# Kernel optimization log

Measured on AMD Instinct MI355X. Metric: run time of the kernel, lower is better.

Reference implementation:

```python
import jax, jax.numpy as jnp
import numpy as np

N_NODES = 100000
N_EDGES = 1600000
N_GRAPHS = 64
HID = 128
N_EXPERTS = 8
IN_DIM = 4


def setup_inputs() -> dict:
    key = jax.random.key(0)
    ks = jax.random.split(key, 12)
    atomic_numbers = jax.random.uniform(ks[0], (N_NODES,), dtype=jnp.float32) * 80.0
    pos = jax.random.normal(ks[1], (N_NODES, 3), dtype=jnp.float32)
    edge_index = jax.random.randint(ks[2], (2, N_EDGES), 0, N_NODES, dtype=jnp.int64)
    batch = jnp.sort(jax.random.randint(ks[3], (N_NODES,), 0, N_GRAPHS, dtype=jnp.int64))
    s1 = 1.0 / np.sqrt(IN_DIM)
    s2 = 1.0 / np.sqrt(HID)
    W1 = jax.random.uniform(ks[4], (IN_DIM, HID), jnp.float32, -s1, s1)
    b1 = jnp.zeros((HID,), jnp.float32)
    W2 = jax.random.uniform(ks[5], (HID, HID), jnp.float32, -s2, s2)
    b2 = jnp.zeros((HID,), jnp.float32)
    Wlin = jax.random.uniform(ks[6], (HID, N_EXPERTS), jnp.float32, -s2, s2)
    blin = jax.random.uniform(ks[7], (N_EXPERTS,), jnp.float32, -s2, s2)
    return {"atomic_numbers": atomic_numbers, "pos": pos, "edge_index": edge_index,
            "batch": batch, "W1": W1, "b1": b1, "W2": W2, "b2": b2,
            "Wlin": Wlin, "blin": blin}


def _gcn_conv(x, W, b, src, dst, deg_inv_sqrt, n_nodes):
    # PyG GCNConv: x' = W x; aggregate deg^-1/2[src]*deg^-1/2[dst] * x'[src] into dst; + bias
    h = x @ W  # [N, out]
    norm = deg_inv_sqrt[src] * deg_inv_sqrt[dst]  # [E+N]
    msg = h[src] * norm[:, None]  # gathered, normalized messages
    out = jax.ops.segment_sum(msg, dst, num_segments=n_nodes)
    return out + b


def reference(atomic_numbers, pos, edge_index, batch, W1, b1, W2, b2, Wlin, blin):
    n = atomic_numbers.shape[0]
    x = jnp.concatenate([atomic_numbers[:, None], pos], axis=-1)  # [N, 4]
    # add self-loops (GCNConv default add_self_loops=True)
    loop = jnp.arange(n, dtype=edge_index.dtype)
    src = jnp.concatenate([edge_index[0], loop])
    dst = jnp.concatenate([edge_index[1], loop])
    deg = jax.ops.segment_sum(jnp.ones_like(dst, dtype=jnp.float32), dst, num_segments=n)
    deg_inv_sqrt = jnp.where(deg > 0, jax.lax.rsqrt(jnp.maximum(deg, 1e-12)), 0.0)
    x = _gcn_conv(x, W1, b1, src, dst, deg_inv_sqrt, n)
    x = jax.nn.relu(x)
    # dropout p=0.5 is identity in eval mode
    x = _gcn_conv(x, W2, b2, src, dst, deg_inv_sqrt, n)
    x = x @ Wlin + blin  # [N, num_experts]
    # global_mean_pool over graph ids
    sums = jax.ops.segment_sum(x, batch, num_segments=N_GRAPHS)
    cnts = jax.ops.segment_sum(jnp.ones((n,), jnp.float32), batch, num_segments=N_GRAPHS)
    pooled = sums / jnp.maximum(cnts, 1.0)[:, None]
    return jax.nn.log_softmax(pooled, axis=1)
```

## Files before the change

### kernel.cpp

```cpp
#include <hip/hip_runtime.h>
#include <math.h>

#define HID 128
#define NEXP 8
#define NGRAPH 64
#define EPC 2048
#define EPT 8
#define MAXB 512
#define NXC 8
#define NREP 8
#define NPS 8
#define HALF 128
#define STAGE_CAP 4096

__device__ inline unsigned short f2bf(float f) {
    unsigned u = __float_as_uint(f);
    u += 0x7FFF + ((u >> 16) & 1);
    return (unsigned short)(u >> 16);
}
__device__ inline unsigned packbf(float lo, float hi) {
    return (unsigned)f2bf(lo) | ((unsigned)f2bf(hi) << 16);
}
__device__ inline float bflo(unsigned u) { return __uint_as_float(u << 16); }
__device__ inline float bfhi(unsigned u) { return __uint_as_float(u & 0xFFFF0000u); }

__global__ void k_init0(float* __restrict__ pool, float* __restrict__ pcnt,
                        const float* __restrict__ W2, const float* __restrict__ Wlin,
                        const float* __restrict__ b2, float* __restrict__ C,
                        float* __restrict__ bb2, int* __restrict__ gcur8,
                        int mregions, int capx) {
    int i = blockIdx.x * 256 + threadIdx.x;
    if (i < mregions) gcur8[i] = i * capx;
    if (i == mregions) gcur8[i] = 0;
    if (i < NREP * NGRAPH * NEXP) pool[i] = 0.0f;
    if (i < NREP * NGRAPH) pcnt[i] = 0.0f;
    int ci = i - NREP * NGRAPH * NEXP;
    if (ci >= 0 && ci < HID * NEXP) {
        int k = ci >> 3, j = ci & 7;
        float s = 0.0f;
        for (int m = 0; m < HID; m++) s += W2[k * HID + m] * Wlin[m * NEXP + j];
        C[ci] = s;
    }
    int bi = ci - HID * NEXP;
    if (bi >= 0 && bi < NEXP) {
        float s = 0.0f;
        for (int m = 0; m < HID; m++) s += b2[m] * Wlin[m * NEXP + bi];
        bb2[bi] = s;
    }
}

__global__ void __launch_bounds__(256) k_binA(
        const int* __restrict__ src, const int* __restrict__ dst,
        int* __restrict__ gcur8, unsigned* __restrict__ binned, int e, int nbuck) {
    __shared__ int h0[MAXB];
    __shared__ int h1[MAXB];
    __shared__ int lstart[MAXB];
    __shared__ int lcur[MAXB];
    __shared__ int gbase[MAXB];
    __shared__ int wtot[4];
    __shared__ unsigned packed[EPC];
    __shared__ unsigned short sbkt[EPC];
    int c = blockIdx.x, t = threadIdx.x;
    int w = t >> 6, lane = t & 63;
    int x = c & (NXC - 1);
    int start = c * EPC;
    int m = e - start < EPC ? e - start : EPC;

    int d[EPT], sv[EPT];
    if (m == EPC) {
        const int4* d4 = (const int4*)(dst + start);
        const int4* s4 = (const int4*)(src + start);
#pragma unroll
        for (int q = 0; q < EPT / 4; q++) {
            int4 dd4 = d4[(EPT / 4) * t + q];
            int4 ss4 = s4[(EPT / 4) * t + q];
            d[4 * q + 0] = dd4.x; d[4 * q + 1] = dd4.y;
            d[4 * q + 2] = dd4.z; d[4 * q + 3] = dd4.w;
            sv[4 * q + 0] = ss4.x; sv[4 * q + 1] = ss4.y;
            sv[4 * q + 2] = ss4.z; sv[4 * q + 3] = ss4.w;
        }
    } else {
#pragma unroll
        for (int j = 0; j < EPT; j++) {
            int idx = t * EPT + j;
            if (idx < m) { d[j] = dst[start + idx]; sv[j] = src[start + idx]; }
        }
    }
    int* hm = (w < 2) ? h0 : h1;
    h0[t] = 0; h0[t + 256] = 0;
    h1[t] = 0; h1[t + 256] = 0;
    __syncthreads();
#pragma unroll
    for (int j = 0; j < EPT; j++)
        if (t * EPT + j < m) atomicAdd(&hm[d[j] >> 8], 1);
    __syncthreads();
    int v0 = h0[2 * t] + h1[2 * t];
    int v1 = h0[2 * t + 1] + h1[2 * t + 1];
    int sum = v0 + v1;
    int incl = sum;
#pragma unroll
    for (int dd = 1; dd < 64; dd <<= 1) {
        int y = __shfl_up(incl, dd, 64);
        if (lane >= dd) incl += y;
    }
    if (lane == 63) wtot[w] = incl;
    __syncthreads();
    int pre = 0;
#pragma unroll
    for (int ww = 0; ww < 4; ww++) pre += (ww < w) ? wtot[ww] : 0;
    int ex = pre + incl - sum;
    lstart[2 * t] = ex;     lstart[2 * t + 1] = ex + v0;
    lcur[2 * t]   = ex;     lcur[2 * t + 1]   = ex + v0;
    for (int b = t; b < nbuck; b += 256) {
        int hv = h0[b] + h1[b];
        gbase[b] = hv ? atomicAdd(&gcur8[b * NXC + x], hv) : 0;
    }
    __syncthreads();
#pragma unroll
    for (int j = 0; j < EPT; j++) {
        if (t * EPT + j < m) {
            int b = d[j] >> 8;
            int p = atomicAdd(&lcur[b], 1);
            packed[p] = ((unsigned)(d[j] & 255) << 24) | (unsigned)sv[j];
            sbkt[p] = (unsigned short)b;
        }
    }
    __syncthreads();
    for (int idx = t; idx < m; idx += 256) {
        int b = sbkt[idx];
        binned[gbase[b] + (idx - lstart[b])] = packed[idx];
    }
}

__global__ void k_binB(const unsigned* __restrict__ binned, const int* __restrict__ gcur8,
                       const float* __restrict__ an, const float* __restrict__ pos,
                       int* __restrict__ cnt, int* __restrict__ off,
                       float* __restrict__ dinv, float4* __restrict__ xs,
                       int* __restrict__ eidx, int n, int capx) {
    __shared__ int h[HALF];
    __shared__ int cur[HALF];
    __shared__ int wtot[2];
    __shared__ int scnt;
    __shared__ unsigned stage[STAGE_CAP];
    int bh = blockIdx.x, t = threadIdx.x;
    int b = bh >> 1, half = bh & 1;
    int cbase = b * NXC;
    int hb = cbase * capx + half * (NXC / 2) * capx;
    int lane = t & 63;
    if (t < HALF) h[t] = 0;
    if (t == 0) scnt = 0;
    __syncthreads();
#pragma unroll
    for (int x = 0; x < NXC; x++) {
        int rs = (cbase + x) * capx, re = gcur8[cbase + x];
        for (int k0 = rs; k0 < re; k0 += 256) {
            int k = k0 + t;
            unsigned u = 0;
            bool keep = false;
            if (k < re) {
                u = binned[k];
                keep = ((int)(u >> 24) >> 7) == half;
            }
            unsigned long long msk = __ballot(keep);
            int pre = __popcll(msk & ((1ull << lane) - 1ull));
            int cw = __popcll(msk);
            int base = 0;
            if (lane == 0 && cw) base = atomicAdd(&scnt, cw);
            base = __shfl(base, 0, 64);
            if (keep) {
                int p = base + pre;
                if (p < STAGE_CAP) stage[p] = u;
                atomicAdd(&h[(u >> 24) & (HALF - 1)], 1);
            }
        }
    }
    __syncthreads();
    int v = 0, ex = 0;
    if (t < HALF) {
        int w = t >> 6;
        v = h[t];
        int incl = v;
#pragma unroll
        for (int dd = 1; dd < 64; dd <<= 1) {
            int y = __shfl_up(incl, dd, 64);
            if (lane >= dd) incl += y;
        }
        if (lane == 63) wtot[w] = incl;
        ex = incl - v;
    }
    __syncthreads();
    if (t < HALF) {
        if (t >= 64) ex += wtot[0];
        cur[t] = ex;
        int node = (b << 8) + half * HALF + t;
        if (node < n) {
            float di = rsqrtf((float)v + 1.0f);
            cnt[node]  = v;
            off[node]  = hb + ex;
            dinv[node] = di;
            xs[node] = make_float4(an[node] * di, pos[3 * node] * di,
                                   pos[3 * node + 1] * di, pos[3 * node + 2] * di);
        }
    }
    __syncthreads();
    int total = scnt < STAGE_CAP ? scnt : STAGE_CAP;
    for (int k = t; k < total; k += 256) {
        unsigned u = stage[k];
        int p = atomicAdd(&cur[(u >> 24) & (HALF - 1)], 1);
        eidx[hb + p] = (int)(u & 0xFFFFFF);
    }
}

__global__ void k_gxz(const float4* __restrict__ xs, const int* __restrict__ eidx,
                      const int* __restrict__ off, const int* __restrict__ cnt,
                      const float* __restrict__ dinv, const float* __restrict__ W1,
                      const float* __restrict__ b1, const float* __restrict__ C,
                      uint4* __restrict__ z, int n) {
    int tid = blockIdx.x * 256 + threadIdx.x;
    int i = tid >> 1;
    int par = tid & 1;
    if (i >= n) return;
    float4 a = par ? make_float4(0.f, 0.f, 0.f, 0.f) : xs[i];
    int o = off[i], c = cnt[i];
    int k = par;
    for (; k + 6 < c; k += 8) {
        int i0 = eidx[o + k],     i1 = eidx[o + k + 2];
        int i2 = eidx[o + k + 4], i3 = eidx[o + k + 6];
        float4 v0 = xs[i0], v1 = xs[i1], v2 = xs[i2], v3 = xs[i3];
        a.x += v0.x + v1.x + v2.x + v3.x;
        a.y += v0.y + v1.y + v2.y + v3.y;
        a.z += v0.z + v1.z + v2.z + v3.z;
        a.w += v0.w + v1.w + v2.w + v3.w;
    }
    for (; k < c; k += 2) {
        float4 v0 = xs[eidx[o + k]];
        a.x += v0.x; a.y += v0.y; a.z += v0.z; a.w += v0.w;
    }
    a.x += __shfl_xor(a.x, 1, 64);
    a.y += __shfl_xor(a.y, 1, 64);
    a.z += __shfl_xor(a.z, 1, 64);
    a.w += __shfl_xor(a.w, 1, 64);
    float di = dinv[i];
    float z0 = 0.f, z1 = 0.f, z2 = 0.f, z3 = 0.f,
          z4 = 0.f, z5 = 0.f, z6 = 0.f, z7 = 0.f;
#pragma unroll 4
    for (int kk = 0; kk < HID; kk++) {
        float x1k = fmaxf(di * (a.x * W1[kk] + a.y * W1[HID + kk] +
                                a.z * W1[2 * HID + kk] + a.w * W1[3 * HID + kk])
                          + b1[kk], 0.0f);
        const float* cr = C + kk * NEXP;
        z0 += x1k * cr[0]; z1 += x1k * cr[1];
        z2 += x1k * cr[2]; z3 += x1k * cr[3];
        z4 += x1k * cr[4]; z5 += x1k * cr[5];
        z6 += x1k * cr[6]; z7 += x1k * cr[7];
    }
    if (par == 0) {
        uint4 outv;
        outv.x = packbf(z0 * di, z1 * di);
        outv.y = packbf(z2 * di, z3 * di);
        outv.z = packbf(z4 * di, z5 * di);
        outv.w = packbf(z6 * di, z7 * di);
        z[i] = outv;
    }
}

__global__ void k_gz(const uint4* __restrict__ z4, const int* __restrict__ eidx,
                     const int* __restrict__ off, const int* __restrict__ cnt,
                     const float* __restrict__ dinv, const int* __restrict__ batch,
                     float* __restrict__ pool, float* __restrict__ pcnt,
                     const float* __restrict__ blin, const float* __restrict__ bb2,
                     float* __restrict__ out, int* __restrict__ ticket,
                     int nblk, int n) {
    int t = threadIdx.x;
    int slot = t >> 4;
    int l = t & 15;
    int i0 = blockIdx.x * (16 * NPS) + slot * NPS;
    if (i0 < n) {
        int i1 = i0 + NPS < n ? i0 + NPS : n;
        int rep = (blockIdx.x + slot) & (NREP - 1);
        float* rp  = pool + (size_t)rep * NGRAPH * NEXP;
        float* rpc = pcnt + (size_t)rep * NGRAPH;
        int Q = l >> 2;

        int curg = -1;
        float r0 = 0.0f, r1 = 0.0f, runlen = 0.0f;
        for (int i = i0; i < i1; i++) {
            float a0 = 0.f, a1 = 0.f, a2 = 0.f, a3 = 0.f,
                  a4 = 0.f, a5 = 0.f, a6 = 0.f, a7 = 0.f;
            int o = off[i], c = cnt[i];
            for (int k = l; k < c; k += 16) {
                uint4 zr = z4[eidx[o + k]];
                a0 += bflo(zr.x); a1 += bfhi(zr.x);
                a2 += bflo(zr.y); a3 += bfhi(zr.y);
                a4 += bflo(zr.z); a5 += bfhi(zr.z);
                a6 += bflo(zr.w); a7 += bfhi(zr.w);
            }
            if (l == 0) {
                uint4 zr = z4[i];
                a0 += bflo(zr.x); a1 += bfhi(zr.x);
                a2 += bflo(zr.y); a3 += bfhi(zr.y);
                a4 += bflo(zr.z); a5 += bfhi(zr.z);
                a6 += bflo(zr.w); a7 += bfhi(zr.w);
            }
            a0 += __shfl_xor(a0, 8, 64); a1 += __shfl_xor(a1, 8, 64);
            a2 += __shfl_xor(a2, 8, 64); a3 += __shfl_xor(a3, 8, 64);
            a4 += __shfl_xor(a4, 8, 64); a5 += __shfl_xor(a5, 8, 64);
            a6 += __shfl_xor(a6, 8, 64); a7 += __shfl_xor(a7, 8, 64);
            a0 += __shfl_xor(a0, 4, 64); a1 += __shfl_xor(a1, 4, 64);
            a2 += __shfl_xor(a2, 4, 64); a3 += __shfl_xor(a3, 4, 64);
            a4 += __shfl_xor(a4, 4, 64); a5 += __shfl_xor(a5, 4, 64);
            a6 += __shfl_xor(a6, 4, 64); a7 += __shfl_xor(a7, 4, 64);
            float r0v, r1v;
            switch (Q) {
                case 0:  r0v = a0; r1v = a1; break;
                case 1:  r0v = a2; r1v = a3; break;
                case 2:  r0v = a4; r1v = a5; break;
                default: r0v = a6; r1v = a7; break;
            }
            r0v += __shfl_xor(r0v, 1, 64); r1v += __shfl_xor(r1v, 1, 64);
            r0v += __shfl_xor(r0v, 2, 64); r1v += __shfl_xor(r1v, 2, 64);
            float di = dinv[i];
            float v0 = di * r0v, v1 = di * r1v;
            int g = batch[i];
            if (g != curg) {
                if (curg >= 0 && (l & 3) == 0) {
                    atomicAdd(&rp[curg * NEXP + 2 * Q], r0);
                    atomicAdd(&rp[curg * NEXP + 2 * Q + 1], r1);
                    if (l == 0) atomicAdd(&rpc[curg], runlen);
                }
                curg = g; r0 = v0; r1 = v1; runlen = 1.0f;
            } else { r0 += v0; r1 += v1; runlen += 1.0f; }
        }
        if (curg >= 0 && (l & 3) == 0) {
            atomicAdd(&rp[curg * NEXP + 2 * Q], r0);
            atomicAdd(&rp[curg * NEXP + 2 * Q + 1], r1);
            if (l == 0) atomicAdd(&rpc[curg], runlen);
        }
    }
    __shared__ int lastFlag;
    __syncthreads();
    if (t == 0) {
        __threadfence();
        lastFlag = (atomicAdd(ticket, 1) == nblk - 1);
    }
    __syncthreads();
    if (lastFlag && t < NGRAPH) {
        int g = t;
        float p[NEXP];
#pragma unroll
        for (int k = 0; k < NEXP; k++) p[k] = 0.0f;
        float cg = 0.0f;
#pragma unroll
        for (int rr = 0; rr < NREP; rr++) {
#pragma unroll
            for (int k = 0; k < NEXP; k++)
                p[k] += atomicAdd(&pool[rr * NGRAPH * NEXP + g * NEXP + k], 0.0f);
            cg += atomicAdd(&pcnt[rr * NGRAPH + g], 0.0f);
        }
        float inv = 1.0f / fmaxf(cg, 1.0f);
        float v[NEXP], m = -1e30f;
#pragma unroll
        for (int k = 0; k < NEXP; k++) {
            v[k] = p[k] * inv + blin[k] + bb2[k];
            m = fmaxf(m, v[k]);
        }
        float s = 0.0f;
#pragma unroll
        for (int k = 0; k < NEXP; k++) s += expf(v[k] - m);
        float ls = logf(s);
#pragma unroll
        for (int k = 0; k < NEXP; k++) out[g * NEXP + k] = v[k] - m - ls;
    }
}

extern "C" void kernel_launch(void* const* d_in, const int* in_sizes, int n_in,
                              void* d_out, int out_size, void* d_ws, size_t ws_size,
                              hipStream_t stream) {
    const float* an   = (const float*)d_in[0];
    const float* pos  = (const float*)d_in[1];
    const int*   ei   = (const int*)d_in[2];
    const int*   batch= (const int*)d_in[3];
    const float* W1   = (const float*)d_in[4];
    const float* b1   = (const float*)d_in[5];
    const float* W2   = (const float*)d_in[6];
    const float* b2   = (const float*)d_in[7];
    const float* Wlin = (const float*)d_in[8];
    const float* blin = (const float*)d_in[9];
    float* out = (float*)d_out;

    const int n = in_sizes[0];
    const int e = in_sizes[2] / 2;
    const int* src = ei;
    const int* dst = ei + e;

    const int nbuck = (n + 255) >> 8;
    const int ch    = (e + EPC - 1) / EPC;
    const int mreg  = nbuck * NXC;
    const int capx  = 2 * (e / (mreg > 0 ? mreg : 1)) + 256;

    char* p = (char*)d_ws;
    float4* xs    = (float4*)p;       p += sizeof(float4) * (size_t)n;
    uint4*  z     = (uint4*)p;        p += sizeof(uint4) * (size_t)n;
    float* C      = (float*)p;        p += sizeof(float) * HID * NEXP;
    float* bb2    = (float*)p;        p += sizeof(float) * NEXP;
    float* dinv   = (float*)p;        p += sizeof(float) * (size_t)n;
    float* pool   = (float*)p;        p += sizeof(float) * NREP * NGRAPH * NEXP;
    float* pcnt   = (float*)p;        p += sizeof(float) * NREP * NGRAPH;
    int*   cnt    = (int*)p;          p += sizeof(int) * (size_t)n;
    int*   off    = (int*)p;          p += sizeof(int) * (size_t)n;
    int*   gcur8  = (int*)p;          p += sizeof(int) * (mreg + 8);
    unsigned* binned = (unsigned*)p;  p += sizeof(unsigned) * (size_t)mreg * capx;
    int*   eidx   = (int*)p;          p += sizeof(int) * (size_t)mreg * capx;
    int*   ticket = gcur8 + mreg;

    const int initN = NREP * NGRAPH * NEXP + HID * NEXP + NEXP;
    const int initG = initN > mreg + 1 ? initN : mreg + 1;
    k_init0<<<(initG + 255) / 256, 256, 0, stream>>>(pool, pcnt, W2, Wlin, b2, C,
                                                     bb2, gcur8, mreg, capx);
    k_binA<<<ch, 256, 0, stream>>>(src, dst, gcur8, binned, e, nbuck);
    k_binB<<<2 * nbuck, 256, 0, stream>>>(binned, gcur8, an, pos, cnt, off, dinv,
                                          xs, eidx, n, capx);

    k_gxz<<<(2 * n + 255) / 256, 256, 0, stream>>>(xs, eidx, off, cnt, dinv,
                                                   W1, b1, C, z, n);

    const int nblk = (n + 16 * NPS - 1) / (16 * NPS);
    k_gz<<<nblk, 256, 0, stream>>>(z, eidx, off, cnt, dinv, batch, pool, pcnt,
                                   blin, bb2, out, ticket, nblk, n);
}
```

Baseline: 206.2 us.

## Enlarge binning chunks and force returning atomics before last-block reduction

The binning kernel now gives each block 6144 edges instead of 2048, with 24 edges per thread. This cuts the number of blocks and the global bucket-offset atomics, but raises register use and shared-memory staging per block. The pooling atomics now use their return values, which forces them to complete before the ticket increment. The threadfence moves from before the ticket to after it, and only the last block executes it. The aim is cheaper ordering at the grid-wide reduction, at some risk to memory-ordering correctness.

```diff
diff --git a/kernel.cpp b/kernel.cpp
--- a/kernel.cpp
+++ b/kernel.cpp
@@ -4,8 +4,7 @@
 #define HID 128
 #define NEXP 8
 #define NGRAPH 64
-#define EPC 2048
-#define EPT 8
+#define EPC 6144
 #define MAXB 512
 #define NXC 8
 #define NREP 8
@@ -66,14 +65,14 @@
     int start = c * EPC;
     int m = e - start < EPC ? e - start : EPC;
 
-    int d[EPT], sv[EPT];
+    int d[24], sv[24];
     if (m == EPC) {
         const int4* d4 = (const int4*)(dst + start);
         const int4* s4 = (const int4*)(src + start);
 #pragma unroll
-        for (int q = 0; q < EPT / 4; q++) {
-            int4 dd4 = d4[(EPT / 4) * t + q];
-            int4 ss4 = s4[(EPT / 4) * t + q];
+        for (int q = 0; q < 6; q++) {
+            int4 dd4 = d4[6 * t + q];
+            int4 ss4 = s4[6 * t + q];
             d[4 * q + 0] = dd4.x; d[4 * q + 1] = dd4.y;
             d[4 * q + 2] = dd4.z; d[4 * q + 3] = dd4.w;
             sv[4 * q + 0] = ss4.x; sv[4 * q + 1] = ss4.y;
@@ -81,8 +80,8 @@
         }
     } else {
 #pragma unroll
-        for (int j = 0; j < EPT; j++) {
-            int idx = t * EPT + j;
+        for (int j = 0; j < 24; j++) {
+            int idx = t * 24 + j;
             if (idx < m) { d[j] = dst[start + idx]; sv[j] = src[start + idx]; }
         }
     }
@@ -91,8 +90,8 @@
     h1[t] = 0; h1[t + 256] = 0;
     __syncthreads();
 #pragma unroll
-    for (int j = 0; j < EPT; j++)
-        if (t * EPT + j < m) atomicAdd(&hm[d[j] >> 8], 1);
+    for (int j = 0; j < 24; j++)
+        if (t * 24 + j < m) atomicAdd(&hm[d[j] >> 8], 1);
     __syncthreads();
     int v0 = h0[2 * t] + h1[2 * t];
     int v1 = h0[2 * t + 1] + h1[2 * t + 1];
@@ -117,8 +116,8 @@
     }
     __syncthreads();
 #pragma unroll
-    for (int j = 0; j < EPT; j++) {
-        if (t * EPT + j < m) {
+    for (int j = 0; j < 24; j++) {
+        if (t * 24 + j < m) {
             int b = d[j] >> 8;
             int p = atomicAdd(&lcur[b], 1);
             packed[p] = ((unsigned)(d[j] & 255) << 24) | (unsigned)sv[j];
@@ -324,52 +323,60 @@
             int g = batch[i];
             if (g != curg) {
                 if (curg >= 0 && (l & 3) == 0) {
-                    atomicAdd(&rp[curg * NEXP + 2 * Q], r0);
-                    atomicAdd(&rp[curg * NEXP + 2 * Q + 1], r1);
-                    if (l == 0) atomicAdd(&rpc[curg], runlen);
+                    float o0 = atomicAdd(&rp[curg * NEXP + 2 * Q], r0);
+                    float o1 = atomicAdd(&rp[curg * NEXP + 2 * Q + 1], r1);
+                    asm volatile("" :: "v"(o0), "v"(o1));
+                    if (l == 0) {
+                        float o2 = atomicAdd(&rpc[curg], runlen);
+                        asm volatile("" :: "v"(o2));
+                    }
                 }
                 curg = g; r0 = v0; r1 = v1; runlen = 1.0f;
             } else { r0 += v0; r1 += v1; runlen += 1.0f; }
         }
         if (curg >= 0 && (l & 3) == 0) {
-            atomicAdd(&rp[curg * NEXP + 2 * Q], r0);
-            atomicAdd(&rp[curg * NEXP + 2 * Q + 1], r1);
-            if (l == 0) atomicAdd(&rpc[curg], runlen);
+            float o0 = atomicAdd(&rp[curg * NEXP + 2 * Q], r0);
+            float o1 = atomicAdd(&rp[curg * NEXP + 2 * Q + 1], r1);
+            asm volatile("" :: "v"(o0), "v"(o1));
+            if (l == 0) {
+                float o2 = atomicAdd(&rpc[curg], runlen);
+                asm volatile("" :: "v"(o2));
+            }
         }
     }
     __shared__ int lastFlag;
     __syncthreads();
-    if (t == 0) {
+    if (t == 0) lastFlag = (atomicAdd(ticket, 1) == nblk - 1);
+    __syncthreads();
+    if (lastFlag) {
         __threadfence();
-        lastFlag = (atomicAdd(ticket, 1) == nblk - 1);
-    }
-    __syncthreads();
-    if (lastFlag && t < NGRAPH) {
-        int g = t;
-        float p[NEXP];
-#pragma unroll
-        for (int k = 0; k < NEXP; k++) p[k] = 0.0f;
-        float cg = 0.0f;
-#pragma unroll
-        for (int rr = 0; rr < NREP; rr++) {
-#pragma unroll
-            for (int k = 0; k < NEXP; k++)
-                p[k] += atomicAdd(&pool[rr * NGRAPH * NEXP + g * NEXP + k], 0.0f);
-            cg += atomicAdd(&pcnt[rr * NGRAPH + g], 0.0f);
-        }
-        float inv = 1.0f / fmaxf(cg, 1.0f);
-        float v[NEXP], m = -1e30f;
-#pragma unroll
-        for (int k = 0; k < NEXP; k++) {
-            v[k] = p[k] * inv + blin[k] + bb2[k];
-            m = fmaxf(m, v[k]);
-        }
-        float s = 0.0f;
-#pragma unroll
-        for (int k = 0; k < NEXP; k++) s += expf(v[k] - m);
-        float ls = logf(s);
-#pragma unroll
-        for (int k = 0; k < NEXP; k++) out[g * NEXP + k] = v[k] - m - ls;
+        if (t < NGRAPH) {
+            int g = t;
+            float p[NEXP];
+#pragma unroll
+            for (int k = 0; k < NEXP; k++) p[k] = 0.0f;
+            float cg = 0.0f;
+#pragma unroll
+            for (int rr = 0; rr < NREP; rr++) {
+#pragma unroll
+                for (int k = 0; k < NEXP; k++)
+                    p[k] += atomicAdd(&pool[rr * NGRAPH * NEXP + g * NEXP + k], 0.0f);
+                cg += atomicAdd(&pcnt[rr * NGRAPH + g], 0.0f);
+            }
+            float inv = 1.0f / fmaxf(cg, 1.0f);
+            float v[NEXP], m = -1e30f;
+#pragma unroll
+            for (int k = 0; k < NEXP; k++) {
+                v[k] = p[k] * inv + blin[k] + bb2[k];
+                m = fmaxf(m, v[k]);
+            }
+            float s = 0.0f;
+#pragma unroll
+            for (int k = 0; k < NEXP; k++) s += expf(v[k] - m);
+            float ls = logf(s);
+#pragma unroll
+            for (int k = 0; k < NEXP; k++) out[g * NEXP + k] = v[k] - m - ls;
+        }
     }
 }
 
```

After: 182.6 us. 1.13x faster.
